# Kernel tuning notes

Hardware: AMD Instinct MI355X
Metric: run time of the kernel (lower is better)

The kernel has to match this reference:

```python
import jax, jax.numpy as jnp
import numpy as np

B, S, D = 4, 2048, 512
H = 8
DH = D // H
NEG = -9e15


def setup_inputs() -> dict:
    key = jax.random.key(0)
    ks = jax.random.split(key, 6)
    x = jax.random.normal(ks[0], (B, S, D), dtype=jnp.float32)
    mask = jax.random.randint(ks[1], (B, S), 0, 2, dtype=jnp.int32)
    # Linear params (torch convention: W [out, in], y = x @ W.T + b)
    lim_qkv = 1.0 / np.sqrt(D)
    W_qkv = jax.random.uniform(ks[2], (3 * D, D), jnp.float32, -lim_qkv, lim_qkv)
    b_qkv = jax.random.uniform(ks[3], (3 * D,), jnp.float32, -lim_qkv, lim_qkv)
    lim_o = 1.0 / np.sqrt(D)
    W_o = jax.random.uniform(ks[4], (D, D), jnp.float32, -lim_o, lim_o)
    b_o = jax.random.uniform(ks[5], (D,), jnp.float32, -lim_o, lim_o)
    return {"x": x, "mask": mask, "W_qkv": W_qkv, "b_qkv": b_qkv, "W_o": W_o, "b_o": b_o}


def reference(x, mask, W_qkv, b_qkv, W_o, b_o):
    b, s, d = x.shape
    # fused QKV projection: [B,S,3D]
    qkv = jnp.einsum('bsd,ed->bse', x, W_qkv) + b_qkv
    qkv = qkv.reshape(b, s, H, 3 * DH).transpose(0, 2, 1, 3)  # [B,H,S,3*DH]
    q, k, v = jnp.split(qkv, 3, axis=-1)  # each [B,H,S,DH]
    logits = jnp.einsum('bhqd,bhkd->bhqk', q, k) / jnp.sqrt(jnp.float32(DH))
    m = mask[:, None, None, :]  # [B,1,1,S]
    logits = jnp.where(m == 0, jnp.float32(NEG), logits)
    attn = jax.nn.softmax(logits, axis=-1)  # [B,H,S,S]
    values = jnp.einsum('bhqk,bhkd->bhqd', attn, v)
    values = values.transpose(0, 2, 1, 3).reshape(b, s, d)
    o = jnp.einsum('bsd,ed->bse', values, W_o) + b_o
    return o
```

## Files before the change

### kernel.cpp

```cpp
#include <hip/hip_runtime.h>
#include <stdint.h>

#define Bv 4
#define Sv 2048
#define Dv 512
#define Hv 8
#define E3 1536
#define PPITCH 164

typedef unsigned short u16;
typedef __bf16 bf16x8 __attribute__((ext_vector_type(8)));
typedef float f32x4 __attribute__((ext_vector_type(4)));

__device__ __forceinline__ u16 f2b(float f) {
  union { float f; uint32_t u; } v; v.f = f;
  uint32_t r = v.u + 0x7FFFu + ((v.u >> 16) & 1u);
  return (u16)(r >> 16);
}

__device__ __forceinline__ void gl_lds16(const void* g, void* l) {
  __builtin_amdgcn_global_load_lds(
      (__attribute__((address_space(1))) void*)(uintptr_t)g,
      (__attribute__((address_space(3))) void*)(uintptr_t)l, 16, 0, 0);
}

__global__ __launch_bounds__(256) void k_cast3(const float* __restrict__ x,
                                               const float* __restrict__ wqkv,
                                               const float* __restrict__ wo,
                                               const int* __restrict__ mask,
                                               u16* __restrict__ xb,
                                               u16* __restrict__ wqkvb,
                                               u16* __restrict__ wob,
                                               float* __restrict__ mbias) {
  const int bid = blockIdx.x;
  if (bid >= 2560) {
    const int i = (bid - 2560) * 256 + threadIdx.x;
    mbias[i] = mask[i] ? 0.0f : -1e30f;
    return;
  }
  const float* in; u16* out; int i;
  if (bid < 2048)      { in = x;    out = xb;    i = bid * 256 + threadIdx.x; }
  else if (bid < 2432) { in = wqkv; out = wqkvb; i = (bid - 2048) * 256 + threadIdx.x; }
  else                 { in = wo;   out = wob;   i = (bid - 2432) * 256 + threadIdx.x; }
  const float4* p = (const float4*)in;
  float4 a = p[(size_t)i * 2], b = p[(size_t)i * 2 + 1];
  union { u16 h[8]; uint4 v; } r;
  r.h[0] = f2b(a.x); r.h[1] = f2b(a.y); r.h[2] = f2b(a.z); r.h[3] = f2b(a.w);
  r.h[4] = f2b(b.x); r.h[5] = f2b(b.y); r.h[6] = f2b(b.z); r.h[7] = f2b(b.w);
  ((uint4*)out)[i] = r.v;
}

template <int OUTF32>
__global__ __launch_bounds__(256) void k_gemm_bt(const u16* __restrict__ A,
                                                 const u16* __restrict__ Bw,
                                                 const float* __restrict__ bias,
                                                 void* __restrict__ C, int N, int K) {
  __shared__ alignas(16) u16 As[128][32];
  __shared__ alignas(16) u16 Bs[128][32];
  const int tid = threadIdx.x, lane = tid & 63, w = tid >> 6;
  const int quad = lane >> 4, l16 = lane & 15;
  const int wm = w & 1, wn = w >> 1;
  const size_t m0 = (size_t)blockIdx.y * 128;
  const int n0 = blockIdx.x * 128;
  const int srow = lane >> 2, scol = (lane & 3) * 8;
  f32x4 acc[4][4] = {};
  for (int k0 = 0; k0 < K; k0 += 32) {
    #pragma unroll
    for (int c = 0; c < 2; ++c) {
      const int rb = (w * 2 + c) * 16;
      gl_lds16(A + (m0 + rb + srow) * K + k0 + scol, &As[rb][0]);
      gl_lds16(Bw + (size_t)(n0 + rb + srow) * K + k0 + scol, &Bs[rb][0]);
    }
    __syncthreads();
    bf16x8 af[4], bfr[4];
    #pragma unroll
    for (int t = 0; t < 4; ++t) {
      af[t]  = *(const bf16x8*)&As[wm * 64 + t * 16 + l16][quad * 8];
      bfr[t] = *(const bf16x8*)&Bs[wn * 64 + t * 16 + l16][quad * 8];
    }
    #pragma unroll
    for (int mt = 0; mt < 4; ++mt)
      #pragma unroll
      for (int nt = 0; nt < 4; ++nt)
        acc[mt][nt] = __builtin_amdgcn_mfma_f32_16x16x32_bf16(af[mt], bfr[nt],
                                                              acc[mt][nt], 0, 0, 0);
    __syncthreads();
  }
  #pragma unroll
  for (int nt = 0; nt < 4; ++nt) {
    const int col = n0 + wn * 64 + nt * 16 + l16;
    const float bv = bias[col];
    #pragma unroll
    for (int mt = 0; mt < 4; ++mt) {
      const size_t row = m0 + wm * 64 + mt * 16 + quad * 4;
      #pragma unroll
      for (int r = 0; r < 4; ++r) {
        float v = acc[mt][nt][r] + bv;
        if (OUTF32) ((float*)C)[(row + r) * N + col] = v;
        else        ((u16*)C)[(row + r) * N + col] = f2b(v);
      }
    }
  }
}

__global__ __launch_bounds__(256) void k_pack(const u16* __restrict__ qkv,
                                              u16* __restrict__ kp,
                                              u16* __restrict__ vp) {
  __shared__ alignas(16) u16 T[64][72];
  const int tid = threadIdx.x;
  const int bh = blockIdx.y, b = bh >> 3, h = bh & 7;
  const int s0 = blockIdx.x * 64;
  const size_t kpb = (size_t)bh * 128 * 1024;
  for (int idx = tid; idx < 512; idx += 256) {
    int r = idx >> 3, c8 = idx & 7;
    uint4 d = *(const uint4*)(qkv + (size_t)(b * Sv + s0 + r) * E3 + h * 192 + 64 + c8 * 8);
    int tile = (s0 >> 4) + (r >> 4), half = c8 >> 2, quad = c8 & 3, l16 = r & 15;
    *(uint4*)(kp + kpb + (size_t)tile * 1024 + half * 512 + (quad * 16 + l16) * 8) = d;
  }
  for (int idx = tid; idx < 512; idx += 256) {
    int r = idx >> 3, c = idx & 7;
    *(uint4*)&T[r][c * 8] =
        *(const uint4*)(qkv + ((size_t)(b * Sv + s0 + r)) * E3 + h * 192 + 128 + c * 8);
  }
  __syncthreads();
  const size_t vpb = (size_t)bh * 64 * 2048;
  for (int idx = tid; idx < 512; idx += 256) {
    int cc = idx >> 8, rest = idx & 255, dh = rest >> 2, kq = rest & 3;
    union { u16 h[8]; uint4 v; } rr;
    #pragma unroll
    for (int j = 0; j < 8; ++j) rr.h[j] = T[cc * 32 + kq * 8 + j][dh];
    int chunk = (s0 >> 5) + cc, nt2 = dh >> 4;
    *(uint4*)(vp + vpb + ((size_t)(chunk * 4 + nt2)) * 512 + (kq * 16 + (dh & 15)) * 8) = rr.v;
  }
}

__global__ __launch_bounds__(256, 4) void k_attn(const u16* __restrict__ qkv,
                                                 const u16* __restrict__ kp,
                                                 const u16* __restrict__ vp,
                                                 const float* __restrict__ mbias,
                                                 u16* __restrict__ vals) {
  __shared__ alignas(16) u16 Ps[4][16 * PPITCH];
  const int tid = threadIdx.x, lane = tid & 63, w = tid >> 6;
  const int quad = lane >> 4, l16 = lane & 15;
  const int bid = blockIdx.x;
  const int bh = bid & 31, strip = bid >> 5;
  const int b = bh >> 3, h = bh & 7;
  const int q0 = strip * 16;

  const u16* qrow = qkv + (size_t)(b * Sv + q0 + l16) * E3 + h * 192 + quad * 8;
  bf16x8 aq0 = *(const bf16x8*)qrow;
  bf16x8 aq1 = *(const bf16x8*)(qrow + 32);

  bf16x8 bones;
  {
    union { u16 u; __bf16 b; } one; one.u = 0x3F80;
    #pragma unroll
    for (int j = 0; j < 8; ++j) bones[j] = one.b;
  }

  f32x4 La = {0.f, 0.f, 0.f, 0.f};
  f32x4 Oa[4] = {};

  const u16* kpb = kp + (size_t)bh * 128 * 1024 + lane * 8;
  const u16* vpb = vp + (size_t)bh * 64 * 2048 + lane * 8;
  const float* mrow = mbias + b * Sv + l16;
  u16* ps_w = &Ps[w][0];
  const float cs = 0.18033688011112042f;
  const int k_begin = w * (Sv / 4), k_end = k_begin + Sv / 4;

  #pragma unroll 1
  for (int k0 = k_begin; k0 < k_end; k0 += 128) {
    const int t0 = k0 >> 4, c0 = k0 >> 5;
    bf16x8 vv[2][4];
    #pragma unroll
    for (int ks = 0; ks < 2; ++ks)
      #pragma unroll
      for (int nt2 = 0; nt2 < 4; ++nt2)
        vv[ks][nt2] = *(const bf16x8*)(vpb + (size_t)((c0 + ks) * 4 + nt2) * 512);
    f32x4 Sa[8] = {};
    #pragma unroll
    for (int nt = 0; nt < 8; ++nt) {
      const u16* tb = kpb + (size_t)(t0 + nt) * 1024;
      bf16x8 bk0 = *(const bf16x8*)tb;
      bf16x8 bk1 = *(const bf16x8*)(tb + 512);
      Sa[nt] = __builtin_amdgcn_mfma_f32_16x16x32_bf16(aq0, bk0, Sa[nt], 0, 0, 0);
      Sa[nt] = __builtin_amdgcn_mfma_f32_16x16x32_bf16(aq1, bk1, Sa[nt], 0, 0, 0);
    }
    #pragma unroll
    for (int nt = 0; nt < 8; ++nt) {
      const float mb = mrow[k0 + nt * 16];
      #pragma unroll
      for (int r = 0; r < 4; ++r) {
        union { float f; uint32_t u; } pv;
        pv.f = __builtin_amdgcn_exp2f(fmaf(Sa[nt][r], cs, mb));
        ps_w[(quad * 4 + r) * PPITCH + nt * 16 + l16] = (u16)(pv.u >> 16);
      }
    }
    bf16x8 vv2[2][4];
    #pragma unroll
    for (int ks = 0; ks < 2; ++ks)
      #pragma unroll
      for (int nt2 = 0; nt2 < 4; ++nt2)
        vv2[ks][nt2] = *(const bf16x8*)(vpb + (size_t)((c0 + 2 + ks) * 4 + nt2) * 512);
    #pragma unroll
    for (int ks = 0; ks < 4; ++ks) {
      bf16x8 ap = *(const bf16x8*)(ps_w + l16 * PPITCH + ks * 32 + quad * 8);
      La = __builtin_amdgcn_mfma_f32_16x16x32_bf16(ap, bones, La, 0, 0, 0);
      #pragma unroll
      for (int nt2 = 0; nt2 < 4; ++nt2) {
        bf16x8 bv8 = (ks < 2) ? vv[ks][nt2] : vv2[ks - 2][nt2];
        Oa[nt2] = __builtin_amdgcn_mfma_f32_16x16x32_bf16(ap, bv8, Oa[nt2], 0, 0, 0);
      }
    }
  }

  if (w != 0) {
    f32x4* fl = (f32x4*)((float*)&Ps[w][0] + lane * 20);
    fl[0] = Oa[0]; fl[1] = Oa[1]; fl[2] = Oa[2]; fl[3] = Oa[3]; fl[4] = La;
  }
  __syncthreads();
  if (w == 0) {
    #pragma unroll
    for (int j = 1; j < 4; ++j) {
      const f32x4* fl = (const f32x4*)((const float*)&Ps[j][0] + lane * 20);
      #pragma unroll
      for (int i = 0; i < 4; ++i) Oa[i] += fl[i];
      La += fl[4];
    }
    float li[4];
    #pragma unroll
    for (int r = 0; r < 4; ++r) li[r] = 1.0f / La[r];
    #pragma unroll
    for (int nt2 = 0; nt2 < 4; ++nt2)
      #pragma unroll
      for (int r = 0; r < 4; ++r) {
        const size_t srow = (size_t)(b * Sv + q0 + quad * 4 + r);
        vals[srow * Dv + h * 64 + nt2 * 16 + l16] = f2b(Oa[nt2][r] * li[r]);
      }
  }
}

extern "C" void kernel_launch(void* const* d_in, const int* in_sizes, int n_in,
                              void* d_out, int out_size, void* d_ws, size_t ws_size,
                              hipStream_t stream) {
  const float* x    = (const float*)d_in[0];
  const int*   mask = (const int*)d_in[1];
  const float* Wqkv = (const float*)d_in[2];
  const float* bqkv = (const float*)d_in[3];
  const float* Wo   = (const float*)d_in[4];
  const float* bo   = (const float*)d_in[5];
  float* out = (float*)d_out;

  char* ws = (char*)d_ws;
  u16* xb    = (u16*)(ws + 0);
  u16* wqkvb = (u16*)(ws + 8388608);
  u16* wob   = (u16*)(ws + 9961472);
  u16* qkv   = (u16*)(ws + 10485760);
  u16* kp    = (u16*)(ws + 35651584);
  u16* vals  = (u16*)(ws + 44040192);
  u16* vp    = (u16*)(ws + 0);
  float* mbias = (float*)(ws + 52428800);

  k_cast3<<<2592, 256, 0, stream>>>(x, Wqkv, Wo, mask, xb, wqkvb, wob, mbias);
  k_gemm_bt<0><<<dim3(12, 64), 256, 0, stream>>>(xb, wqkvb, bqkv, qkv, E3, Dv);
  k_pack<<<dim3(32, 32), 256, 0, stream>>>(qkv, kp, vp);
  k_attn<<<4096, 256, 0, stream>>>(qkv, kp, vp, mbias, vals);
  k_gemm_bt<1><<<dim3(4, 64), 256, 0, stream>>>(vals, wob, bo, out, Dv, Dv);
}
```

Baseline: 202.6 us.

## Keep attention probabilities in registers via transposed QK^T and repacked V layout

Swaps the QK^T MFMA operands so each lane holds scores for one query across keys. The bf16 probabilities can then be packed in registers and fed straight into the PV MFMA as a half-filled K=32 operand, with no round trip through LDS. V is pre-permuted into a matching per-16-key tile layout. The row sum is kept as a scalar and reduced with shuffles, which drops the ones-vector MFMA. In exchange, the PV MFMAs use only half their K depth, so twice as many PV MFMA instructions are issued.

New measurement: 223.6 us. 10.4% more time.

```diff
diff --git a/kernel.cpp b/kernel.cpp
--- a/kernel.cpp
+++ b/kernel.cpp
@@ -6,7 +6,6 @@
 #define Dv 512
 #define Hv 8
 #define E3 1536
-#define PPITCH 164
 
 typedef unsigned short u16;
 typedef __bf16 bf16x8 __attribute__((ext_vector_type(8)));
@@ -123,14 +122,14 @@
         *(const uint4*)(qkv + ((size_t)(b * Sv + s0 + r)) * E3 + h * 192 + 128 + c * 8);
   }
   __syncthreads();
-  const size_t vpb = (size_t)bh * 64 * 2048;
-  for (int idx = tid; idx < 512; idx += 256) {
-    int cc = idx >> 8, rest = idx & 255, dh = rest >> 2, kq = rest & 3;
-    union { u16 h[8]; uint4 v; } rr;
-    #pragma unroll
-    for (int j = 0; j < 8; ++j) rr.h[j] = T[cc * 32 + kq * 8 + j][dh];
-    int chunk = (s0 >> 5) + cc, nt2 = dh >> 4;
-    *(uint4*)(vp + vpb + ((size_t)(chunk * 4 + nt2)) * 512 + (kq * 16 + (dh & 15)) * 8) = rr.v;
+  const size_t vpb = (size_t)bh * 128 * 1024;
+  for (int idx = tid; idx < 1024; idx += 256) {
+    int tl = idx >> 8, rest = idx & 255, nt2 = rest >> 6, ln = rest & 63;
+    int q = ln >> 4, l16 = ln & 15;
+    union { u16 h[4]; uint2 v; } rr;
+    #pragma unroll
+    for (int j = 0; j < 4; ++j) rr.h[j] = T[tl * 16 + q * 4 + j][nt2 * 16 + l16];
+    *(uint2*)(vp + vpb + ((size_t)((s0 >> 4) + tl)) * 1024 + ln * 16 + nt2 * 4) = rr.v;
   }
 }
 
@@ -139,7 +138,8 @@
                                                  const u16* __restrict__ vp,
                                                  const float* __restrict__ mbias,
                                                  u16* __restrict__ vals) {
-  __shared__ alignas(16) u16 Ps[4][16 * PPITCH];
+  __shared__ float fbuf[3][64 * 20];
+  __shared__ float lsbuf[16];
   const int tid = threadIdx.x, lane = tid & 63, w = tid >> 6;
   const int quad = lane >> 4, l16 = lane & 15;
   const int bid = blockIdx.x;
@@ -151,85 +151,84 @@
   bf16x8 aq0 = *(const bf16x8*)qrow;
   bf16x8 aq1 = *(const bf16x8*)(qrow + 32);
 
-  bf16x8 bones;
-  {
-    union { u16 u; __bf16 b; } one; one.u = 0x3F80;
-    #pragma unroll
-    for (int j = 0; j < 8; ++j) bones[j] = one.b;
-  }
-
-  f32x4 La = {0.f, 0.f, 0.f, 0.f};
+  float ls = 0.f;
   f32x4 Oa[4] = {};
 
   const u16* kpb = kp + (size_t)bh * 128 * 1024 + lane * 8;
-  const u16* vpb = vp + (size_t)bh * 64 * 2048 + lane * 8;
-  const float* mrow = mbias + b * Sv + l16;
-  u16* ps_w = &Ps[w][0];
+  const u16* vpb = vp + (size_t)bh * 128 * 1024 + lane * 16;
+  const float* mbase = mbias + b * Sv;
   const float cs = 0.18033688011112042f;
   const int k_begin = w * (Sv / 4), k_end = k_begin + Sv / 4;
 
   #pragma unroll 1
   for (int k0 = k_begin; k0 < k_end; k0 += 128) {
-    const int t0 = k0 >> 4, c0 = k0 >> 5;
-    bf16x8 vv[2][4];
-    #pragma unroll
-    for (int ks = 0; ks < 2; ++ks)
-      #pragma unroll
-      for (int nt2 = 0; nt2 < 4; ++nt2)
-        vv[ks][nt2] = *(const bf16x8*)(vpb + (size_t)((c0 + ks) * 4 + nt2) * 512);
+    const int t0 = k0 >> 4;
     f32x4 Sa[8] = {};
     #pragma unroll
     for (int nt = 0; nt < 8; ++nt) {
       const u16* tb = kpb + (size_t)(t0 + nt) * 1024;
       bf16x8 bk0 = *(const bf16x8*)tb;
       bf16x8 bk1 = *(const bf16x8*)(tb + 512);
-      Sa[nt] = __builtin_amdgcn_mfma_f32_16x16x32_bf16(aq0, bk0, Sa[nt], 0, 0, 0);
-      Sa[nt] = __builtin_amdgcn_mfma_f32_16x16x32_bf16(aq1, bk1, Sa[nt], 0, 0, 0);
-    }
+      Sa[nt] = __builtin_amdgcn_mfma_f32_16x16x32_bf16(bk0, aq0, Sa[nt], 0, 0, 0);
+      Sa[nt] = __builtin_amdgcn_mfma_f32_16x16x32_bf16(bk1, aq1, Sa[nt], 0, 0, 0);
+    }
+    uint32_t pk0[8], pk1[8];
     #pragma unroll
     for (int nt = 0; nt < 8; ++nt) {
-      const float mb = mrow[k0 + nt * 16];
-      #pragma unroll
-      for (int r = 0; r < 4; ++r) {
-        union { float f; uint32_t u; } pv;
-        pv.f = __builtin_amdgcn_exp2f(fmaf(Sa[nt][r], cs, mb));
-        ps_w[(quad * 4 + r) * PPITCH + nt * 16 + l16] = (u16)(pv.u >> 16);
-      }
-    }
-    bf16x8 vv2[2][4];
-    #pragma unroll
-    for (int ks = 0; ks < 2; ++ks)
-      #pragma unroll
-      for (int nt2 = 0; nt2 < 4; ++nt2)
-        vv2[ks][nt2] = *(const bf16x8*)(vpb + (size_t)((c0 + 2 + ks) * 4 + nt2) * 512);
-    #pragma unroll
-    for (int ks = 0; ks < 4; ++ks) {
-      bf16x8 ap = *(const bf16x8*)(ps_w + l16 * PPITCH + ks * 32 + quad * 8);
-      La = __builtin_amdgcn_mfma_f32_16x16x32_bf16(ap, bones, La, 0, 0, 0);
-      #pragma unroll
-      for (int nt2 = 0; nt2 < 4; ++nt2) {
-        bf16x8 bv8 = (ks < 2) ? vv[ks][nt2] : vv2[ks - 2][nt2];
-        Oa[nt2] = __builtin_amdgcn_mfma_f32_16x16x32_bf16(ap, bv8, Oa[nt2], 0, 0, 0);
-      }
-    }
-  }
+      const float4 mb4 = *(const float4*)(mbase + k0 + nt * 16 + quad * 4);
+      union { float f; uint32_t u; } p0, p1, p2, p3;
+      p0.f = __builtin_amdgcn_exp2f(fmaf(Sa[nt][0], cs, mb4.x));
+      p1.f = __builtin_amdgcn_exp2f(fmaf(Sa[nt][1], cs, mb4.y));
+      p2.f = __builtin_amdgcn_exp2f(fmaf(Sa[nt][2], cs, mb4.z));
+      p3.f = __builtin_amdgcn_exp2f(fmaf(Sa[nt][3], cs, mb4.w));
+      ls += (p0.f + p1.f) + (p2.f + p3.f);
+      pk0[nt] = __builtin_amdgcn_perm(p1.u + 0x8000u, p0.u + 0x8000u, 0x07060302u);
+      pk1[nt] = __builtin_amdgcn_perm(p3.u + 0x8000u, p2.u + 0x8000u, 0x07060302u);
+    }
+    #pragma unroll
+    for (int nt = 0; nt < 8; ++nt) {
+      const uint4 vA = *(const uint4*)(vpb + (size_t)(t0 + nt) * 1024);
+      const uint4 vB = *(const uint4*)(vpb + (size_t)(t0 + nt) * 1024 + 8);
+      union { uint32_t d[4]; bf16x8 v; } af, b0, b1, b2, b3;
+      af.d[0] = pk0[nt]; af.d[1] = pk1[nt]; af.d[2] = 0; af.d[3] = 0;
+      b0.d[0] = vA.x; b0.d[1] = vA.y; b0.d[2] = 0; b0.d[3] = 0;
+      b1.d[0] = vA.z; b1.d[1] = vA.w; b1.d[2] = 0; b1.d[3] = 0;
+      b2.d[0] = vB.x; b2.d[1] = vB.y; b2.d[2] = 0; b2.d[3] = 0;
+      b3.d[0] = vB.z; b3.d[1] = vB.w; b3.d[2] = 0; b3.d[3] = 0;
+      Oa[0] = __builtin_amdgcn_mfma_f32_16x16x32_bf16(af.v, b0.v, Oa[0], 0, 0, 0);
+      Oa[1] = __builtin_amdgcn_mfma_f32_16x16x32_bf16(af.v, b1.v, Oa[1], 0, 0, 0);
+      Oa[2] = __builtin_amdgcn_mfma_f32_16x16x32_bf16(af.v, b2.v, Oa[2], 0, 0, 0);
+      Oa[3] = __builtin_amdgcn_mfma_f32_16x16x32_bf16(af.v, b3.v, Oa[3], 0, 0, 0);
+    }
+  }
+
+  ls += __shfl_xor(ls, 16);
+  ls += __shfl_xor(ls, 32);
 
   if (w != 0) {
-    f32x4* fl = (f32x4*)((float*)&Ps[w][0] + lane * 20);
-    fl[0] = Oa[0]; fl[1] = Oa[1]; fl[2] = Oa[2]; fl[3] = Oa[3]; fl[4] = La;
+    float* fl = &fbuf[w - 1][lane * 20];
+    *(f32x4*)(fl + 0)  = Oa[0];
+    *(f32x4*)(fl + 4)  = Oa[1];
+    *(f32x4*)(fl + 8)  = Oa[2];
+    *(f32x4*)(fl + 12) = Oa[3];
+    fl[16] = ls;
   }
   __syncthreads();
   if (w == 0) {
     #pragma unroll
-    for (int j = 1; j < 4; ++j) {
-      const f32x4* fl = (const f32x4*)((const float*)&Ps[j][0] + lane * 20);
-      #pragma unroll
-      for (int i = 0; i < 4; ++i) Oa[i] += fl[i];
-      La += fl[4];
-    }
+    for (int j = 0; j < 3; ++j) {
+      const float* fl = &fbuf[j][lane * 20];
+      Oa[0] += *(const f32x4*)(fl + 0);
+      Oa[1] += *(const f32x4*)(fl + 4);
+      Oa[2] += *(const f32x4*)(fl + 8);
+      Oa[3] += *(const f32x4*)(fl + 12);
+      ls += fl[16];
+    }
+    if (quad == 0) lsbuf[l16] = ls;
+    const f32x4 lt = *(const f32x4*)&lsbuf[quad * 4];
     float li[4];
     #pragma unroll
-    for (int r = 0; r < 4; ++r) li[r] = 1.0f / La[r];
+    for (int r = 0; r < 4; ++r) li[r] = 1.0f / lt[r];
     #pragma unroll
     for (int nt2 = 0; nt2 < 4; ++nt2)
       #pragma unroll
```

## Fuse K/V packing into QKV GEMM epilogue and retile output GEMM

Applied to the files above, without the earlier changes.

The QKV projection epilogue now scatters its results directly into separate Q, packed-K and packed-V buffers in the MFMA-friendly layouts attention expects. This removes the separate pack kernel and its extra read and write of the QKV intermediate. The output projection gets a dedicated kernel with 64-row tiles, doubling the block count for better CU occupancy. The trade-off is scalar 2-byte scattered stores in the epilogue, which may coalesce poorly.

Result: no change. 204.1 us (+0.8%).

```diff
diff --git a/kernel.cpp b/kernel.cpp
--- a/kernel.cpp
+++ b/kernel.cpp
@@ -6,7 +6,6 @@
 #define Dv 512
 #define Hv 8
 #define E3 1536
-#define PPITCH 164
 
 typedef unsigned short u16;
 typedef __bf16 bf16x8 __attribute__((ext_vector_type(8)));
@@ -50,11 +49,13 @@
   ((uint4*)out)[i] = r.v;
 }
 
-template <int OUTF32>
-__global__ __launch_bounds__(256) void k_gemm_bt(const u16* __restrict__ A,
-                                                 const u16* __restrict__ Bw,
-                                                 const float* __restrict__ bias,
-                                                 void* __restrict__ C, int N, int K) {
+__global__ __launch_bounds__(256) void k_gemm_qkv(const u16* __restrict__ A,
+                                                  const u16* __restrict__ Bw,
+                                                  const float* __restrict__ bias,
+                                                  u16* __restrict__ qp,
+                                                  u16* __restrict__ kp,
+                                                  u16* __restrict__ vp) {
+  const int K = Dv, N = E3;
   __shared__ alignas(16) u16 As[128][32];
   __shared__ alignas(16) u16 Bs[128][32];
   const int tid = threadIdx.x, lane = tid & 63, w = tid >> 6;
@@ -88,53 +89,83 @@
   }
   #pragma unroll
   for (int nt = 0; nt < 4; ++nt) {
-    const int col = n0 + wn * 64 + nt * 16 + l16;
+    const int cbase = n0 + wn * 64 + nt * 16;
+    const int h = cbase / 192, rem = cbase % 192;
+    const int region = rem >> 6;
+    const int dh = (rem & 63) + l16;
+    const float bv = bias[cbase + l16];
+    #pragma unroll
+    for (int mt = 0; mt < 4; ++mt) {
+      #pragma unroll
+      for (int r = 0; r < 4; ++r) {
+        const int row = (int)m0 + wm * 64 + mt * 16 + quad * 4 + r;
+        const u16 vb = f2b(acc[mt][nt][r] + bv);
+        const int b = row >> 11, s = row & 2047;
+        const size_t bhb = ((size_t)(b * 8 + h)) * 131072;
+        if (region == 0) {
+          qp[(size_t)row * 512 + h * 64 + dh] = vb;
+        } else if (region == 1) {
+          kp[bhb + (s >> 4) * 1024 + (dh >> 5) * 512 + ((dh >> 3) & 3) * 128 +
+             (s & 15) * 8 + (dh & 7)] = vb;
+        } else {
+          vp[bhb + (s >> 5) * 2048 + (dh >> 4) * 512 + ((s >> 3) & 3) * 128 +
+             (dh & 15) * 8 + (s & 7)] = vb;
+        }
+      }
+    }
+  }
+}
+
+__global__ __launch_bounds__(256) void k_gemm_out(const u16* __restrict__ A,
+                                                  const u16* __restrict__ Bw,
+                                                  const float* __restrict__ bias,
+                                                  float* __restrict__ C) {
+  const int K = Dv, N = Dv;
+  __shared__ alignas(16) u16 As[64][32];
+  __shared__ alignas(16) u16 Bs[128][32];
+  const int tid = threadIdx.x, lane = tid & 63, w = tid >> 6;
+  const int quad = lane >> 4, l16 = lane & 15;
+  const size_t m0 = (size_t)blockIdx.y * 64;
+  const int n0 = blockIdx.x * 128;
+  const int srow = lane >> 2, scol = (lane & 3) * 8;
+  f32x4 acc[4][2] = {};
+  for (int k0 = 0; k0 < K; k0 += 32) {
+    gl_lds16(A + (m0 + w * 16 + srow) * K + k0 + scol, &As[w * 16][0]);
+    #pragma unroll
+    for (int c = 0; c < 2; ++c) {
+      const int rb = w * 32 + c * 16;
+      gl_lds16(Bw + (size_t)(n0 + rb + srow) * K + k0 + scol, &Bs[rb][0]);
+    }
+    __syncthreads();
+    bf16x8 af[4], bfr[2];
+    #pragma unroll
+    for (int t = 0; t < 4; ++t) af[t] = *(const bf16x8*)&As[t * 16 + l16][quad * 8];
+    #pragma unroll
+    for (int t = 0; t < 2; ++t)
+      bfr[t] = *(const bf16x8*)&Bs[w * 32 + t * 16 + l16][quad * 8];
+    #pragma unroll
+    for (int mt = 0; mt < 4; ++mt)
+      #pragma unroll
+      for (int nt = 0; nt < 2; ++nt)
+        acc[mt][nt] = __builtin_amdgcn_mfma_f32_16x16x32_bf16(af[mt], bfr[nt],
+                                                              acc[mt][nt], 0, 0, 0);
+    __syncthreads();
+  }
+  #pragma unroll
+  for (int nt = 0; nt < 2; ++nt) {
+    const int col = n0 + w * 32 + nt * 16 + l16;
     const float bv = bias[col];
     #pragma unroll
     for (int mt = 0; mt < 4; ++mt) {
-      const size_t row = m0 + wm * 64 + mt * 16 + quad * 4;
-      #pragma unroll
-      for (int r = 0; r < 4; ++r) {
-        float v = acc[mt][nt][r] + bv;
-        if (OUTF32) ((float*)C)[(row + r) * N + col] = v;
-        else        ((u16*)C)[(row + r) * N + col] = f2b(v);
-      }
-    }
-  }
-}
-
-__global__ __launch_bounds__(256) void k_pack(const u16* __restrict__ qkv,
-                                              u16* __restrict__ kp,
-                                              u16* __restrict__ vp) {
-  __shared__ alignas(16) u16 T[64][72];
-  const int tid = threadIdx.x;
-  const int bh = blockIdx.y, b = bh >> 3, h = bh & 7;
-  const int s0 = blockIdx.x * 64;
-  const size_t kpb = (size_t)bh * 128 * 1024;
-  for (int idx = tid; idx < 512; idx += 256) {
-    int r = idx >> 3, c8 = idx & 7;
-    uint4 d = *(const uint4*)(qkv + (size_t)(b * Sv + s0 + r) * E3 + h * 192 + 64 + c8 * 8);
-    int tile = (s0 >> 4) + (r >> 4), half = c8 >> 2, quad = c8 & 3, l16 = r & 15;
-    *(uint4*)(kp + kpb + (size_t)tile * 1024 + half * 512 + (quad * 16 + l16) * 8) = d;
-  }
-  for (int idx = tid; idx < 512; idx += 256) {
-    int r = idx >> 3, c = idx & 7;
-    *(uint4*)&T[r][c * 8] =
-        *(const uint4*)(qkv + ((size_t)(b * Sv + s0 + r)) * E3 + h * 192 + 128 + c * 8);
-  }
-  __syncthreads();
-  const size_t vpb = (size_t)bh * 64 * 2048;
-  for (int idx = tid; idx < 512; idx += 256) {
-    int cc = idx >> 8, rest = idx & 255, dh = rest >> 2, kq = rest & 3;
-    union { u16 h[8]; uint4 v; } rr;
-    #pragma unroll
-    for (int j = 0; j < 8; ++j) rr.h[j] = T[cc * 32 + kq * 8 + j][dh];
-    int chunk = (s0 >> 5) + cc, nt2 = dh >> 4;
-    *(uint4*)(vp + vpb + ((size_t)(chunk * 4 + nt2)) * 512 + (kq * 16 + (dh & 15)) * 8) = rr.v;
-  }
-}
-
-__global__ __launch_bounds__(256, 4) void k_attn(const u16* __restrict__ qkv,
+      const size_t row = m0 + mt * 16 + quad * 4;
+      #pragma unroll
+      for (int r = 0; r < 4; ++r) C[(row + r) * N + col] = acc[mt][nt][r] + bv;
+    }
+  }
+}
+
+#define PPITCH 164
+__global__ __launch_bounds__(256, 4) void k_attn(const u16* __restrict__ qp,
                                                  const u16* __restrict__ kp,
                                                  const u16* __restrict__ vp,
                                                  const float* __restrict__ mbias,
@@ -147,7 +178,7 @@
   const int b = bh >> 3, h = bh & 7;
   const int q0 = strip * 16;
 
-  const u16* qrow = qkv + (size_t)(b * Sv + q0 + l16) * E3 + h * 192 + quad * 8;
+  const u16* qrow = qp + (size_t)(b * Sv + q0 + l16) * 512 + h * 64 + quad * 8;
   bf16x8 aq0 = *(const bf16x8*)qrow;
   bf16x8 aq1 = *(const bf16x8*)(qrow + 32);
 
@@ -161,8 +192,8 @@
   f32x4 La = {0.f, 0.f, 0.f, 0.f};
   f32x4 Oa[4] = {};
 
-  const u16* kpb = kp + (size_t)bh * 128 * 1024 + lane * 8;
-  const u16* vpb = vp + (size_t)bh * 64 * 2048 + lane * 8;
+  const u16* kpb = kp + (size_t)bh * 131072 + lane * 8;
+  const u16* vpb = vp + (size_t)bh * 131072 + lane * 8;
   const float* mrow = mbias + b * Sv + l16;
   u16* ps_w = &Ps[w][0];
   const float cs = 0.18033688011112042f;
@@ -255,15 +286,14 @@
   u16* xb    = (u16*)(ws + 0);
   u16* wqkvb = (u16*)(ws + 8388608);
   u16* wob   = (u16*)(ws + 9961472);
-  u16* qkv   = (u16*)(ws + 10485760);
-  u16* kp    = (u16*)(ws + 35651584);
-  u16* vals  = (u16*)(ws + 44040192);
-  u16* vp    = (u16*)(ws + 0);
-  float* mbias = (float*)(ws + 52428800);
+  u16* qp    = (u16*)(ws + 10485760);
+  u16* kp    = (u16*)(ws + 18874368);
+  u16* vp    = (u16*)(ws + 27262976);
+  u16* vals  = (u16*)(ws + 35651584);
+  float* mbias = (float*)(ws + 44040192);
 
   k_cast3<<<2592, 256, 0, stream>>>(x, Wqkv, Wo, mask, xb, wqkvb, wob, mbias);
-  k_gemm_bt<0><<<dim3(12, 64), 256, 0, stream>>>(xb, wqkvb, bqkv, qkv, E3, Dv);
-  k_pack<<<dim3(32, 32), 256, 0, stream>>>(qkv, kp, vp);
-  k_attn<<<4096, 256, 0, stream>>>(qkv, kp, vp, mbias, vals);
-  k_gemm_bt<1><<<dim3(4, 64), 256, 0, stream>>>(vals, wob, bo, out, Dv, Dv);
-}
+  k_gemm_qkv<<<dim3(12, 64), 256, 0, stream>>>(xb, wqkvb, bqkv, qp, kp, vp);
+  k_attn<<<4096, 256, 0, stream>>>(qp, kp, vp, mbias, vals);
+  k_gemm_out<<<dim3(4, 128), 256, 0, stream>>>(vals, wob, bo, out);
+}
```
